# Kernel optimization log

Hardware: AMD Instinct MI355X
Metric: run time of the kernel (lower is better)

The kernel has to match this reference:

```python
import jax, jax.numpy as jnp
import numpy as np

B, D, R = 2048, 512, 32  # batch, in_dim, num_relations


def setup_inputs() -> dict:
    key = jax.random.key(0)
    k1, k2, k3, k4, k5 = jax.random.split(key, 5)
    return {
        "head_emb": jax.random.normal(k1, (B, D), dtype=jnp.float32),
        "tail_emb": jax.random.normal(k2, (B, D), dtype=jnp.float32),
        "rel_id": jax.random.randint(k3, (B,), 0, R, dtype=jnp.int32),
        "W": jax.random.normal(k4, (R, D, D), dtype=jnp.float32),
        "b": jax.random.normal(k5, (R, D), dtype=jnp.float32),
    }


def reference(head_emb, tail_emb, rel_id, W, b):
    # Per-sample relation gather: W_r [B, D, D], b_r [B, D]
    W_r = W[rel_id]
    b_r = b[rel_id]
    # tail @ W_r^T per sample: proj[b, e] = sum_d tail[b, d] * W_r[b, e, d]
    proj = jnp.einsum('bd,bed->be', tail_emb, W_r)
    # score[b] = sum_e head[b, e] * proj[b, e] + b_r[b, e]
    score = jnp.sum(head_emb * proj + b_r, axis=1)
    return score
```

## Files before the change

### kernel.cpp

```cpp
#include <hip/hip_runtime.h>
#include <hip/hip_bf16.h>

#define BB 2048
#define DD 512
#define RR 32

#define NB 64
#define KB 128
#define KS 32
#define NKS (KB / KS)
#define MT 96
#define SLCAP 256
#define NPART 32

#define A_STRIDE 132

typedef __attribute__((ext_vector_type(8))) short bf16x8;
typedef __attribute__((ext_vector_type(4))) float f32x4;

__device__ __forceinline__ unsigned cvt_pk(float a, float b) {
    union { __hip_bfloat162 h2; unsigned u; } c;
    c.h2 = __float22bfloat162_rn(make_float2(a, b));
    return c.u;
}

template <int CTRL>
__device__ __forceinline__ float ror_add(float v) {
    int t = __builtin_amdgcn_update_dpp(0, __float_as_int(v), CTRL, 0xf, 0xf, true);
    return v + __int_as_float(t);
}
__device__ __forceinline__ float row16_sum(float v) {
    v = ror_add<0x128>(v);
    v = ror_add<0x124>(v);
    v = ror_add<0x122>(v);
    v = ror_add<0x121>(v);
    return v;
}

__launch_bounds__(256, 4)
__global__ void k_main(const float* __restrict__ head,
                       const float* __restrict__ tail,
                       const int* __restrict__ rel,
                       const float* __restrict__ W,
                       const float* __restrict__ b,
                       float* __restrict__ part) {
    const int bid = blockIdx.x;
    const int x = bid & 7, p = bid >> 3;
    const int r  = (x << 2) | (p >> 5);
    const int nc = (p >> 2) & 7;
    const int kc = p & 3;
    const int e0 = nc * NB;
    const int k0 = kc * KB;
    const int jplane = (nc << 2) | kc;
    const int tid = threadIdx.x;
    const int wave = tid >> 6;
    const int lane = tid & 63;
    const int l15 = lane & 15, lg = lane >> 4;

    __shared__ unsigned short A_lds[MT * A_STRIDE];
    __shared__ int slist[SLCAP];
    __shared__ float scpart[MT];
    __shared__ int cntS;
    __shared__ float bsS;

    if (tid == 0) cntS = 0;
    __syncthreads();

    const int4* rp = (const int4*)rel;
    int4 rv0 = rp[tid * 2 + 0];
    int4 rv1 = rp[tid * 2 + 1];
    float bv = (wave == 0) ? b[r * DD + e0 + lane] : 0.f;

    const float* Wrow = W + ((size_t)r * DD + e0 + wave * 16 + l15) * DD + k0 + lg * 8;
    float4 wv[NKS][2];
    #pragma unroll
    for (int ks = 0; ks < NKS; ks++) {
        wv[ks][0] = *(const float4*)(Wrow + ks * KS);
        wv[ks][1] = *(const float4*)(Wrow + ks * KS + 4);
    }

    {
        int base = tid * 8;
        if (rv0.x == r) { int q = atomicAdd(&cntS, 1); if (q < SLCAP) slist[q] = base; }
        if (rv0.y == r) { int q = atomicAdd(&cntS, 1); if (q < SLCAP) slist[q] = base + 1; }
        if (rv0.z == r) { int q = atomicAdd(&cntS, 1); if (q < SLCAP) slist[q] = base + 2; }
        if (rv0.w == r) { int q = atomicAdd(&cntS, 1); if (q < SLCAP) slist[q] = base + 3; }
        if (rv1.x == r) { int q = atomicAdd(&cntS, 1); if (q < SLCAP) slist[q] = base + 4; }
        if (rv1.y == r) { int q = atomicAdd(&cntS, 1); if (q < SLCAP) slist[q] = base + 5; }
        if (rv1.z == r) { int q = atomicAdd(&cntS, 1); if (q < SLCAP) slist[q] = base + 6; }
        if (rv1.w == r) { int q = atomicAdd(&cntS, 1); if (q < SLCAP) slist[q] = base + 7; }
    }
    {
        float v = bv;
        v = row16_sum(v);
        v += __shfl_xor(v, 16);
        v += __shfl_xor(v, 32);
        if (wave == 0 && lane == 0) bsS = v;
    }

    asm volatile("s_waitcnt lgkmcnt(0)" ::: "memory");
    __builtin_amdgcn_s_barrier();
    __builtin_amdgcn_sched_barrier(0);

    const int n = min(cntS, SLCAP);
    const float biasv = (kc == 0) ? bsS : 0.f;
    const int ebase = e0 + wave * 16;

    bf16x8 bfr[NKS];
    bool converted = false;

    for (int ts = 0; ts < n; ts += MT) {
        const int tn = min(MT, n - ts);
        if (ts > 0) __syncthreads();
        if (tid < MT) scpart[tid] = biasv;

        float hreg[MT / 16][4];
        #pragma unroll
        for (int m = 0; m < MT / 16; m++) {
            #pragma unroll
            for (int q = 0; q < 4; q++) {
                int sl = m * 16 + lg * 4 + q;
                int si = min(sl, tn - 1);
                hreg[m][q] = head[(size_t)slist[ts + si] * DD + ebase + l15];
            }
        }

        #pragma unroll
        for (int i = 0; i < (MT * KB / 4) / 256; i++) {
            int idx = i * 256 + tid;
            int row = idx >> 5, fc = idx & 31;
            float4 v = make_float4(0.f, 0.f, 0.f, 0.f);
            if (row < tn)
                v = *(const float4*)(tail + (size_t)slist[ts + row] * DD + k0 + fc * 4);
            unsigned* pa = (unsigned*)&A_lds[row * A_STRIDE + fc * 4];
            pa[0] = cvt_pk(v.x, v.y);
            pa[1] = cvt_pk(v.z, v.w);
        }
        __syncthreads();

        if (!converted) {
            #pragma unroll
            for (int ks = 0; ks < NKS; ks++) {
                union { unsigned u[4]; bf16x8 v; } bb;
                bb.u[0] = cvt_pk(wv[ks][0].x, wv[ks][0].y);
                bb.u[1] = cvt_pk(wv[ks][0].z, wv[ks][0].w);
                bb.u[2] = cvt_pk(wv[ks][1].x, wv[ks][1].y);
                bb.u[3] = cvt_pk(wv[ks][1].z, wv[ks][1].w);
                bfr[ks] = bb.v;
            }
            converted = true;
        }

        f32x4 acc[MT / 16];
        #pragma unroll
        for (int m = 0; m < MT / 16; m++) acc[m] = (f32x4){0.f, 0.f, 0.f, 0.f};

        #pragma unroll
        for (int ks = 0; ks < NKS; ks++) {
            #pragma unroll
            for (int m = 0; m < MT / 16; m++) {
                bf16x8 af = *(const bf16x8*)&A_lds[(m * 16 + l15) * A_STRIDE + ks * KS + lg * 8];
                acc[m] = __builtin_amdgcn_mfma_f32_16x16x32_bf16(af, bfr[ks], acc[m], 0, 0, 0);
            }
        }

        #pragma unroll
        for (int m = 0; m < MT / 16; m++) {
            #pragma unroll
            for (int q = 0; q < 4; q++) {
                int sl = m * 16 + lg * 4 + q;
                float v = acc[m][q] * hreg[m][q];
                v = row16_sum(v);
                if (l15 == 0 && sl < tn) atomicAdd(&scpart[sl], v);
            }
        }
        __syncthreads();
        if (tid < tn) part[(size_t)slist[ts + tid] * NPART + jplane] = scpart[tid];
    }
}

__global__ void k_reduce(const float* __restrict__ part, float* __restrict__ out) {
    int i = blockIdx.x * 256 + threadIdx.x;
    const float4* p = (const float4*)(part + (size_t)i * NPART);
    float s = 0.f;
    #pragma unroll
    for (int j = 0; j < NPART / 4; j++) {
        float4 v = p[j];
        s += v.x + v.y + v.z + v.w;
    }
    out[i] = s;
}

extern "C" void kernel_launch(void* const* d_in, const int* in_sizes, int n_in,
                              void* d_out, int out_size, void* d_ws, size_t ws_size,
                              hipStream_t stream) {
    const float* head = (const float*)d_in[0];
    const float* tail = (const float*)d_in[1];
    const int*   rel  = (const int*)d_in[2];
    const float* W    = (const float*)d_in[3];
    const float* b    = (const float*)d_in[4];
    float* out  = (float*)d_out;
    float* part = (float*)d_ws;

    k_main<<<RR * (DD / NB) * (DD / KB), 256, 0, stream>>>(head, tail, rel, W, b, part);
    k_reduce<<<BB / 256, 256, 0, stream>>>(part, out);
}
```

Before: 21.24 us.

## Fuse partial-score reduction into main kernel via last-block-per-relation counter

```diff
diff --git a/kernel.cpp b/kernel.cpp
--- a/kernel.cpp
+++ b/kernel.cpp
@@ -43,7 +43,9 @@
                        const int* __restrict__ rel,
                        const float* __restrict__ W,
                        const float* __restrict__ b,
-                       float* __restrict__ part) {
+                       float* __restrict__ part,
+                       int* __restrict__ cnt,
+                       float* __restrict__ out) {
     const int bid = blockIdx.x;
     const int x = bid & 7, p = bid >> 3;
     const int r  = (x << 2) | (p >> 5);
@@ -62,6 +64,7 @@
     __shared__ float scpart[MT];
     __shared__ int cntS;
     __shared__ float bsS;
+    __shared__ int lastS;
 
     if (tid == 0) cntS = 0;
     __syncthreads();
@@ -175,20 +178,23 @@
             }
         }
         __syncthreads();
-        if (tid < tn) part[(size_t)slist[ts + tid] * NPART + jplane] = scpart[tid];
-    }
-}
-
-__global__ void k_reduce(const float* __restrict__ part, float* __restrict__ out) {
-    int i = blockIdx.x * 256 + threadIdx.x;
-    const float4* p = (const float4*)(part + (size_t)i * NPART);
-    float s = 0.f;
-    #pragma unroll
-    for (int j = 0; j < NPART / 4; j++) {
-        float4 v = p[j];
-        s += v.x + v.y + v.z + v.w;
-    }
-    out[i] = s;
+        if (tid < tn)
+            atomicExch(&part[(size_t)slist[ts + tid] * NPART + jplane], scpart[tid]);
+    }
+
+    __syncthreads();
+    if (tid == 0) lastS = (atomicAdd(&cnt[r], 1) == NPART - 1);
+    __syncthreads();
+    if (lastS) {
+        for (int s = tid; s < n; s += 256) {
+            float* ps = part + (size_t)slist[s] * NPART;
+            float acc = 0.f;
+            #pragma unroll
+            for (int j = 0; j < NPART; j++)
+                acc += atomicAdd(&ps[j], 0.f);
+            out[slist[s]] = acc;
+        }
+    }
 }
 
 extern "C" void kernel_launch(void* const* d_in, const int* in_sizes, int n_in,
@@ -201,7 +207,9 @@
     const float* b    = (const float*)d_in[4];
     float* out  = (float*)d_out;
     float* part = (float*)d_ws;
-
-    k_main<<<RR * (DD / NB) * (DD / KB), 256, 0, stream>>>(head, tail, rel, W, b, part);
-    k_reduce<<<BB / 256, 256, 0, stream>>>(part, out);
-}
+    int*   cnt  = (int*)((char*)d_ws + (size_t)BB * NPART * sizeof(float));
+
+    hipMemsetAsync(cnt, 0, RR * sizeof(int), stream);
+    k_main<<<RR * (DD / NB) * (DD / KB), 256, 0, stream>>>(head, tail, rel, W, b,
+                                                           part, cnt, out);
+}
```

Measured after the change: 39.78 us. +87.3%, slower.
